# Optimization experiments

Measured on AMD Instinct MI355X. Metric: run time of the kernel, lower is better.

The kernel has to match this reference:

```python
import jax, jax.numpy as jnp
import numpy as np

L_DEG = 4      # max out-degree L
DEPTH = 7      # complete L-ary tree depth -> 21845 nodes
N_GEN = 16
C_ST = 8
M_LAB = 256


def _build_tree():
    sizes = [L_DEG ** d for d in range(DEPTH + 1)]
    limits = np.concatenate([[0], np.cumsum(sizes)]).astype(np.int64)
    t_size = int(limits[-1])
    nodes = np.arange(t_size)
    rng = np.random.default_rng(0)
    labels = rng.integers(0, M_LAB, t_size)
    parent = np.where(nodes > 0, (nodes - 1) // L_DEG, 0)
    pos = np.where(nodes > 0, (nodes - 1) % L_DEG, 0)
    ch = np.zeros((t_size, L_DEG), dtype=np.int64)
    n_internal = int(limits[-2])
    ch[:n_internal] = L_DEG * nodes[:n_internal, None] + np.arange(1, L_DEG + 1)[None, :]
    t = np.concatenate([labels[:, None], parent[:, None], pos[:, None], ch], axis=1).astype(np.int64)
    return t, limits


def setup_inputs() -> dict:
    key = jax.random.key(0)
    ka, kb, kp, ks = jax.random.split(key, 4)
    t, limits = _build_tree()
    return {
        "t": jnp.asarray(t),
        "t_limits": jnp.asarray(limits),
        "a": jax.random.normal(ka, (N_GEN, C_ST, C_ST, L_DEG), dtype=jnp.float32),
        "b": jax.random.normal(kb, (N_GEN, C_ST, M_LAB), dtype=jnp.float32),
        "pi": jax.random.normal(kp, (N_GEN, C_ST, L_DEG), dtype=jnp.float32),
        "sp": jax.random.normal(ks, (N_GEN, L_DEG), dtype=jnp.float32),
    }


def _forward(tn, lim, a, b, pi, sp):
    # tn, lim are host numpy int arrays (tree structure is a constant).
    G, C, _, L = a.shape
    t_size = int(lim[-1])
    n_levels = len(lim) - 1
    sL = int(lim[-2])                      # first leaf index
    labels = tn[:, 0]
    posf = tn[:, 2]
    ch_all = tn[:, 3:3 + L]

    sm_a = jax.nn.softmax(a, axis=1)       # P(parent_state i | child_state j, pos l)
    sm_b = jax.nn.softmax(b, axis=2)
    sm_pi = jax.nn.softmax(pi, axis=1)
    sm_sp = jax.nn.softmax(sp, axis=1)
    a_sp = sm_a * sm_sp[:, None, None, :]  # [G,i,j,L]

    # ---------------- upward pass ----------------
    prior = jnp.zeros((t_size, G, C), a.dtype)
    beta = jnp.zeros((t_size, G, C), a.dtype)
    beta_il = jnp.zeros((t_size, G, C), a.dtype)

    prior_lv = jnp.moveaxis(sm_pi[:, :, posf[sL:]], 2, 0)   # [NL,G,C]
    emis_lv = jnp.moveaxis(sm_b[:, :, labels[sL:]], 2, 0)   # [NL,G,C]
    beta_lv = prior_lv * emis_lv
    beta_lv = beta_lv / jnp.sum(beta_lv, axis=2, keepdims=True)
    prior = prior.at[sL:].set(prior_lv)
    beta = beta.at[sL:].set(beta_lv)

    for lev in range(n_levels - 2, -1, -1):   # internal levels, bottom-up
        s, e = int(lim[lev]), int(lim[lev + 1])
        ch = ch_all[s:e]                       # [P,L]
        mask = (ch > 0).astype(a.dtype)        # children packed in first slots
        prior_ch = prior[ch]                   # [P,L,G,C]
        beta_ch = beta[ch]                     # [P,L,G,C]
        u_prior = jnp.einsum('gijl,pl,plgj->pgi', a_sp, mask, prior_ch)
        u_bil = jnp.einsum('gijl,pl,plgj->pgi', a_sp, mask, beta_ch) / u_prior
        emis = jnp.moveaxis(sm_b[:, :, labels[s:e]], 2, 0)  # [P,G,C]
        tmp = emis * u_bil * u_prior
        u_beta = tmp / jnp.sum(tmp, axis=2, keepdims=True)
        prior = prior.at[s:e].set(u_prior)
        beta = beta.at[s:e].set(u_beta)
        beta_il = beta_il.at[s:e].set(u_bil)

    # ---------------- downward pass ----------------
    # row t_size is a dummy slot for padded (absent) children
    eps_i = jnp.zeros((t_size + 1, G, C), a.dtype).at[0].set(beta[0])
    eps_ijl = jnp.zeros((t_size, G, C, C, L), a.dtype)
    for lev in range(0, n_levels - 1):         # parents, top-down (root included)
        s, e = int(lim[lev]), int(lim[lev + 1])
        ch = ch_all[s:e]
        maskb = ch > 0
        mask = maskb.astype(a.dtype)
        beta_ch = jnp.transpose(beta[ch], (0, 2, 3, 1))       # [P,G,Cj,L]
        pe = eps_i[s:e] / (prior[s:e] * beta_il[s:e])         # [P,G,Ci]
        res = (pe[:, :, :, None, None] * a_sp[None]
               * beta_ch[:, :, None, :, :]
               * mask[:, None, None, None, :])                # [P,G,i,j,L]
        child_eps = jnp.sum(res, axis=3)                       # sum over j (as in source) -> [P,G,i,L]
        vals = jnp.moveaxis(child_eps, 3, 1).reshape(-1, G, C) # [P*L,G,C]
        safe = np.where(maskb, ch, t_size).reshape(-1)
        eps_i = eps_i.at[safe].set(vals)
        eps_ijl = eps_ijl.at[s:e].set(res)
    eps_i = eps_i[:t_size]
    # leaves' eps_ijl stay zero (source scatters zeros there)

    # ---------------- log-likelihood ----------------
    a_lh = jnp.einsum('ugijl,gijl->g', eps_ijl, jnp.log(sm_a))
    b_lh = jnp.einsum('ugc,gcu->g', eps_i, jnp.log(sm_b)[:, :, labels])
    pi_lh = jnp.einsum('ugc,gcu->g', eps_i[sL:], jnp.log(sm_pi)[:, :, posf[sL:]])
    eps_l = jnp.sum(eps_ijl, axis=(2, 3))                      # [u,g,L]
    sp_lh = jnp.einsum('ugl,gl->g', eps_l, jnp.log(sm_sp))
    return a_lh + b_lh + pi_lh + sp_lh


def reference(t, t_limits, a, b, pi, sp):
    tn = np.asarray(t)
    lim = np.asarray(t_limits)
    return _forward(tn, lim, a, b, pi, sp)
```

## Files before the change

kernel.cpp:

```cpp
#include <hip/hip_runtime.h>


#define G 16
#define C 8
#define GC 128
#define TSIZE 21845
#define SL 5461

__device__ __forceinline__ float grp8_sum(float v) {
  v += __shfl_xor(v, 1);
  v += __shfl_xor(v, 2);
  v += __shfl_xor(v, 4);
  return v;
}

__global__ void setup_kernel(const float* __restrict__ ain, const float* __restrict__ bin,
                             const float* __restrict__ piin, const float* __restrict__ spin,
                             float* __restrict__ a_sp, float* __restrict__ log_a,
                             float* __restrict__ sm_bT, float* __restrict__ log_bT,
                             float* __restrict__ sm_piT, float* __restrict__ log_piT,
                             float* __restrict__ log_sp, float* __restrict__ out) {
  int blk = blockIdx.x, tid = threadIdx.x;
  if (blk < 16) {
    int g = blk;
    __shared__ float red4[4];
    for (int c = 0; c < 8; ++c) {
      int row = g * 8 + c;
      float x = bin[row * 256 + tid];
      float m = x;
      #pragma unroll
      for (int off2 = 32; off2; off2 >>= 1) m = fmaxf(m, __shfl_xor(m, off2));
      if ((tid & 63) == 0) red4[tid >> 6] = m;
      __syncthreads();
      m = fmaxf(fmaxf(red4[0], red4[1]), fmaxf(red4[2], red4[3]));
      __syncthreads();
      float e = expf(x - m);
      float ssum = e;
      #pragma unroll
      for (int off2 = 32; off2; off2 >>= 1) ssum += __shfl_xor(ssum, off2);
      if ((tid & 63) == 0) red4[tid >> 6] = ssum;
      __syncthreads();
      ssum = red4[0] + red4[1] + red4[2] + red4[3];
      __syncthreads();
      sm_bT[tid * GC + row]  = e / ssum;
      log_bT[tid * GC + row] = (x - m) - logf(ssum);
    }
  } else if (blk == 16) {
    for (int col = tid; col < 512; col += 256) {
      int g = col >> 5, j = (col >> 2) & 7, l = col & 3;
      float x[8], m = -1e30f;
      #pragma unroll
      for (int i = 0; i < 8; ++i) { x[i] = ain[g*256 + i*32 + j*4 + l]; m = fmaxf(m, x[i]); }
      float ssum = 0.f;
      #pragma unroll
// ... 7 lines not shown
      for (int i = 0; i < 8; ++i) {
        int o2 = g*256 + i*32 + j*4 + l;
        float smv = expf(x[i] - m) / ssum;
        a_sp[o2]  = smv * spv;
        log_a[o2] = (x[i] - m) - ls;
      }
    }
  } else {
    if (tid < 64) {
      int g = tid >> 2, l = tid & 3;
      float x[8], m = -1e30f;
      #pragma unroll
      for (int c = 0; c < 8; ++c) { x[c] = piin[g*32 + c*4 + l]; m = fmaxf(m, x[c]); }
      float ssum = 0.f;
      #pragma unroll
      for (int c = 0; c < 8; ++c) ssum += expf(x[c] - m);
      float ls = logf(ssum);
      #pragma unroll
      for (int c = 0; c < 8; ++c) {
        sm_piT[l*GC + g*8 + c]  = expf(x[c] - m) / ssum;
        log_piT[l*GC + g*8 + c] = (x[c] - m) - ls;
      }
    } else if (tid < 80) {
      int g = tid - 64;
      float y[4], m = -1e30f;
      #pragma unroll
      for (int l = 0; l < 4; ++l) { y[l] = spin[g*4 + l]; m = fmaxf(m, y[l]); }
      float ssum = 0.f;
      #pragma unroll
      for (int l = 0; l < 4; ++l) ssum += expf(y[l] - m);
      float ls = logf(ssum);
      #pragma unroll
      for (int l = 0; l < 4; ++l) log_sp[g*4 + l] = (y[l] - m) - ls;
    } else if (tid >= 128 && tid < 144) {
      out[tid - 128] = 0.0f;
    }
  }
}

__device__ __forceinline__ void up_lds(int v, int lab, int gi, int g8,
    const float* asp, const float* __restrict__ sm_bT,
    float* sBeta, float* sNum, bool wantNum) {
  int ch0 = 4*v + 1;
  float ub = 0.f;
  #pragma unroll
  for (int l = 0; l < 4; ++l) {
    const float4* bp = (const float4*)(sBeta + (ch0 + l)*GC + g8);
    float4 b0 = bp[0], b1 = bp[1];
    ub += asp[l]*b0.x + asp[4+l]*b0.y + asp[8+l]*b0.z + asp[12+l]*b0.w
        + asp[16+l]*b1.x + asp[20+l]*b1.y + asp[24+l]*b1.z + asp[28+l]*b1.w;
  }
  float tmp = sm_bT[lab*GC + gi] * ub;
  float s = grp8_sum(tmp);
  sBeta[v*GC + gi] = tmp / s;
  if (wantNum) sNum[v*GC + gi] = ub;
}

__device__ __forceinline__ double down_lds(int v, int lab, float e, int gi, int g8,
    const float* asp, const float* aal, const float* lsp,
    const float* __restrict__ log_bT, float* sBeta, const float* sNum) {
  float pe = e / sNum[v*GC + gi];
  int ch0 = 4*v + 1;
  float local = 0.f;
  #pragma unroll
  for (int l = 0; l < 4; ++l) {
    float4* bp = (float4*)(sBeta + (ch0 + l)*GC + g8);
    float4 b0 = bp[0], b1 = bp[1];
    float S = asp[l]*b0.x + asp[4+l]*b0.y + asp[8+l]*b0.z + asp[12+l]*b0.w
            + asp[16+l]*b1.x + asp[20+l]*b1.y + asp[24+l]*b1.z + asp[28+l]*b1.w;
    float A = aal[l]*b0.x + aal[4+l]*b0.y + aal[8+l]*b0.z + aal[12+l]*b0.w
            + aal[16+l]*b1.x + aal[20+l]*b1.y + aal[24+l]*b1.z + aal[28+l]*b1.w;
    float ce = pe * S;
    sBeta[(ch0 + l)*GC + gi] = ce;
    local += pe*A + ce*lsp[l];
  }
  return (double)local + (double)(e * log_bT[lab*GC + gi]);
}

__device__ __forceinline__ void up_g(int u, int lab, int gi, int g8,
    const float* asp, const float* __restrict__ sm_bT,
    float* __restrict__ betaG, float* __restrict__ numG) {
  int ch0 = 4*u + 1;
  float ub = 0.f;
  #pragma unroll
  for (int l = 0; l < 4; ++l) {
    const float4* bp = (const float4*)(betaG + (size_t)(ch0 + l)*GC + g8);
    float4 b0 = bp[0], b1 = bp[1];
    ub += asp[l]*b0.x + asp[4+l]*b0.y + asp[8+l]*b0.z + asp[12+l]*b0.w
        + asp[16+l]*b1.x + asp[20+l]*b1.y + asp[24+l]*b1.z + asp[28+l]*b1.w;
  }
  float tmp = sm_bT[lab*GC + gi] * ub;
  float s = grp8_sum(tmp);
  betaG[(size_t)u*GC + gi] = tmp / s;
  numG[(size_t)u*GC + gi]  = ub;
}

__device__ __forceinline__ double down_g(int u, int lab, int gi, int g8,
    const float* asp, const float* aal, const float* lsp,
    const float* __restrict__ log_bT, const float* __restrict__ numG,
    const float* __restrict__ betaG, float* __restrict__ epsG) {
  float e  = epsG[(size_t)u*GC + gi];
  float pe = e / numG[(size_t)u*GC + gi];
  int ch0 = 4*u + 1;
  float local = 0.f;
  #pragma unroll
  for (int l = 0; l < 4; ++l) {
    const float4* bp = (const float4*)(betaG + (size_t)(ch0 + l)*GC + g8);
    float4 b0 = bp[0], b1 = bp[1];
    float S = asp[l]*b0.x + asp[4+l]*b0.y + asp[8+l]*b0.z + asp[12+l]*b0.w
            + asp[16+l]*b1.x + asp[20+l]*b1.y + asp[24+l]*b1.z + asp[28+l]*b1.w;
    float A = aal[l]*b0.x + aal[4+l]*b0.y + aal[8+l]*b0.z + aal[12+l]*b0.w
            + aal[16+l]*b1.x + aal[20+l]*b1.y + aal[24+l]*b1.z + aal[28+l]*b1.w;
    float ce = pe * S;
    epsG[(size_t)(ch0 + l)*GC + gi] = ce;
    local += pe*A + ce*lsp[l];
  }
  return (double)local + (double)(e * log_bT[lab*GC + gi]);
}

__global__ __launch_bounds__(1024, 1) void up_kernel(
    const float* __restrict__ a_sp, const float* __restrict__ sm_bT,
    const float* __restrict__ sm_piT, const int* __restrict__ t,
    float* __restrict__ betaG) {
  __shared__ float sBeta[85*GC];
  const int blk = blockIdx.x, tid = threadIdx.x;
  const int gi = tid & 127, g = gi >> 3, i = gi & 7, g8 = g*8, w = tid >> 7;
  float asp[32];
  {
    const float4* pa = (const float4*)(a_sp + g*256 + i*32);
    #pragma unroll
    for (int q = 0; q < 8; ++q) {
      float4 v = pa[q];
      asp[q*4+0]=v.x; asp[q*4+1]=v.y; asp[q*4+2]=v.z; asp[q*4+3]=v.w;
    }
  }
  const int base_leaf = SL + blk*64;
  #pragma unroll
  for (int it = 0; it < 8; ++it) {
    int k = it*8 + w;
    float bt = sm_piT[(k & 3)*GC + gi] * sm_bT[t[(base_leaf + k)*7]*GC + gi];
    float s = grp8_sum(bt);
    sBeta[(21 + k)*GC + gi] = bt / s;
  }
  __syncthreads();
  #pragma unroll
  for (int it = 0; it < 2; ++it) {
    int k = it*8 + w;
    up_lds(5 + k, t[(1365 + blk*16 + k)*7], gi, g8, asp, sm_bT, sBeta, nullptr, false);
  }
  __syncthreads();
  if (tid < 512)
    up_lds(1 + w, t[(341 + blk*4 + w)*7], gi, g8, asp, sm_bT, sBeta, nullptr, false);
  __syncthreads();
  if (tid < 128) {
    up_lds(0, t[(85 + blk)*7], gi, g8, asp, sm_bT, sBeta, nullptr, false);
    betaG[(size_t)(85 + blk)*GC + gi] = sBeta[gi];
  }
}

__global__ __launch_bounds__(512, 2) void top_kernel(
    const float* __restrict__ a_sp, const float* __restrict__ log_a,
    const float* __restrict__ log_sp, const float* __restrict__ sm_bT,
    const float* __restrict__ log_bT, const int* __restrict__ t,
    float* __restrict__ betaG, float* __restrict__ numG,
    float* __restrict__ epsG, float* __restrict__ out) {
  int g = blockIdx.x, tid = threadIdx.x;
  int i = tid & 7, gi = g*8 + i, q = tid >> 3, g8 = g*8;
  float asp[32], aal[32], lsp[4];
  {
    const float4* pa = (const float4*)(a_sp + g*256 + i*32);
    const float4* pl = (const float4*)(log_a + g*256 + i*32);
    #pragma unroll
    for (int k = 0; k < 8; ++k) {
      float4 va = pa[k], vl = pl[k];
      asp[k*4+0]=va.x; asp[k*4+1]=va.y; asp[k*4+2]=va.z; asp[k*4+3]=va.w;
      aal[k*4+0]=va.x*vl.x; aal[k*4+1]=va.y*vl.y; aal[k*4+2]=va.z*vl.z; aal[k*4+3]=va.w*vl.w;
    }
    #pragma unroll
    for (int l = 0; l < 4; ++l) lsp[l] = log_sp[g*4 + l];
  }
  up_g(21 + q, t[(21 + q)*7], gi, g8, asp, sm_bT, betaG, numG);
  __syncthreads();
  if (tid < 128) up_g(5 + q, t[(5 + q)*7], gi, g8, asp, sm_bT, betaG, numG);
  __syncthreads();
  if (tid < 32)  up_g(1 + q, t[(1 + q)*7], gi, g8, asp, sm_bT, betaG, numG);
  __syncthreads();
  if (tid < 8) {
    up_g(0, t[0], gi, g8, asp, sm_bT, betaG, numG);
    epsG[gi] = betaG[gi];
  }
  __syncthreads();
  double acc = 0.0;
  if (tid < 8)
    acc += down_g(0, t[0], gi, g8, asp, aal, lsp, log_bT, numG, betaG, epsG);
  __syncthreads();
  if (tid < 32)
    acc += down_g(1 + q, t[(1 + q)*7], gi, g8, asp, aal, lsp, log_bT, numG, betaG, epsG);
  __syncthreads();
  if (tid < 128)
    acc += down_g(5 + q, t[(5 + q)*7], gi, g8, asp, aal, lsp, log_bT, numG, betaG, epsG);
  __syncthreads();
  acc += down_g(21 + q, t[(21 + q)*7], gi, g8, asp, aal, lsp, log_bT, numG, betaG, epsG);
  acc += __shfl_xor(acc, 1);
  acc += __shfl_xor(acc, 2);
  acc += __shfl_xor(acc, 4);
  __shared__ double sd[64];
  if (i == 0) sd[q] = acc;
  __syncthreads();
  if (tid == 0) {
    double s = 0.0;
    for (int k = 0; k < 64; ++k) s += sd[k];
    atomicAdd(&out[g], (float)s);
  }
}

__global__ __launch_bounds__(1024, 1) void down_kernel(
    const float* __restrict__ a_sp, const float* __restrict__ log_a,
    const float* __restrict__ log_sp, const float* __restrict__ sm_bT,
    const float* __restrict__ log_bT, const float* __restrict__ sm_piT,
    const float* __restrict__ log_piT, const int* __restrict__ t,
    const float* __restrict__ epsG, float* __restrict__ out) {
  __shared__ float  sBeta[85*GC];
  __shared__ float  sNum[21*GC];
  __shared__ double sd[128];
  const int blk = blockIdx.x, tid = threadIdx.x;
  const int gi = tid & 127, g = gi >> 3, i = gi & 7, g8 = g*8, w = tid >> 7;
  float asp[32], aal[32], lsp[4];
  {
    const float4* pa = (const float4*)(a_sp  + g*256 + i*32);
    const float4* pl = (const float4*)(log_a + g*256 + i*32);
    #pragma unroll
    for (int k = 0; k < 8; ++k) {
      float4 va = pa[k], vl = pl[k];
      asp[k*4+0]=va.x; asp[k*4+1]=va.y; asp[k*4+2]=va.z; asp[k*4+3]=va.w;
      aal[k*4+0]=va.x*vl.x; aal[k*4+1]=va.y*vl.y; aal[k*4+2]=va.z*vl.z; aal[k*4+3]=va.w*vl.w;
    }
    #pragma unroll
    for (int l = 0; l < 4; ++l) lsp[l] = log_sp[g*4 + l];
  }
  const int base_leaf = SL + blk*64;
  #pragma unroll
  for (int it = 0; it < 8; ++it) {
    int k = it*8 + w;
    float bt = sm_piT[(k & 3)*GC + gi] * sm_bT[t[(base_leaf + k)*7]*GC + gi];
    float s = grp8_sum(bt);
    sBeta[(21 + k)*GC + gi] = bt / s;
  }
  __syncthreads();
  #pragma unroll
  for (int it = 0; it < 2; ++it) {
    int k = it*8 + w;
    up_lds(5 + k, t[(1365 + blk*16 + k)*7], gi, g8, asp, sm_bT, sBeta, sNum, true);
  }
  __syncthreads();
  if (tid < 512)
    up_lds(1 + w, t[(341 + blk*4 + w)*7], gi, g8, asp, sm_bT, sBeta, sNum, true);
  __syncthreads();
  double acc = 0.0;
  if (tid < 128) {
    up_lds(0, t[(85 + blk)*7], gi, g8, asp, sm_bT, sBeta, sNum, true);
    float e = epsG[(size_t)(85 + blk)*GC + gi];
    acc += down_lds(0, t[(85 + blk)*7], e, gi, g8, asp, aal, lsp, log_bT, sBeta, sNum);
  }
  __syncthreads();
  if (tid < 512) {
    int v = 1 + w;
    float e = sBeta[v*GC + gi];
    acc += down_lds(v, t[(341 + blk*4 + w)*7], e, gi, g8, asp, aal, lsp, log_bT, sBeta, sNum);
  }
  __syncthreads();
  #pragma unroll
  for (int it = 0; it < 2; ++it) {
    int k = it*8 + w, v = 5 + k;
    float e = sBeta[v*GC + gi];
    acc += down_lds(v, t[(1365 + blk*16 + k)*7], e, gi, g8, asp, aal, lsp, log_bT, sBeta, sNum);
  }
  __syncthreads();
  #pragma unroll
  for (int it = 0; it < 8; ++it) {
    int k = it*8 + w;
    float e = sBeta[(21 + k)*GC + gi];
    acc += (double)(e * (log_bT[t[(base_leaf + k)*7]*GC + gi] +
                         log_piT[(k & 3)*GC + gi]));
  }
  acc += __shfl_xor(acc, 1);
  acc += __shfl_xor(acc, 2);
  acc += __shfl_xor(acc, 4);
  if (i == 0) sd[tid >> 3] = acc;
  __syncthreads();
  if (tid < 16) {
    double s = 0.0;
    #pragma unroll
    for (int c = 0; c < 8; ++c) s += sd[tid + 16*c];
    atomicAdd(&out[tid], (float)s);
  }
}

extern "C" void kernel_launch(void* const* d_in, const int* in_sizes, int n_in,
                              void* d_out, int out_size, void* d_ws, size_t ws_size,
                              hipStream_t stream) {
  const int*   t  = (const int*)d_in[0];
  const float* a  = (const float*)d_in[2];
  const float* b  = (const float*)d_in[3];
  const float* pi = (const float*)d_in[4];
  const float* sp = (const float*)d_in[5];
  float* out = (float*)d_out;

  char* w = (char*)d_ws;
  size_t off = 0;
  auto carve = [&](size_t bytes) -> void* {
    void* ptr = w + off;
    off += (bytes + 255) & ~(size_t)255;
    return ptr;
  };
  float* a_sp    = (float*)carve((size_t)16*8*8*4*4);
  float* log_a   = (float*)carve((size_t)16*8*8*4*4);
  float* sm_bT   = (float*)carve((size_t)256*GC*4);
  float* log_bT  = (float*)carve((size_t)256*GC*4);
  float* sm_piT  = (float*)carve((size_t)4*GC*4);
  float* log_piT = (float*)carve((size_t)4*GC*4);
  float* log_sp  = (float*)carve((size_t)16*4*4);
  float* betaG   = (float*)carve((size_t)341*GC*4);
  float* numG    = (float*)carve((size_t)85*GC*4);
  float* epsG    = (float*)carve((size_t)341*GC*4);

  setup_kernel<<<18, 256, 0, stream>>>(a, b, pi, sp, a_sp, log_a, sm_bT, log_bT,
                                       sm_piT, log_piT, log_sp, out);
  up_kernel<<<256, 1024, 0, stream>>>(a_sp, sm_bT, sm_piT, t, betaG);
  top_kernel<<<16, 512, 0, stream>>>(a_sp, log_a, log_sp, sm_bT, log_bT, t,
                                     betaG, numG, epsG, out);
  down_kernel<<<256, 1024, 0, stream>>>(a_sp, log_a, log_sp, sm_bT, log_bT,
                                        sm_piT, log_piT, t, epsG, out);
}
```

Measured before the change: 116.6 us.

## Fuse up, top and down kernels into one persistent kernel with grid sync

Replaces the separate up, top and down kernels with a single 256-block kernel. Blocks publish their subtree roots, and the last block to arrive (found with an atomic counter) runs the top-of-tree pass while the other blocks spin-wait on a flag. This removes two kernel launches and the recomputation of the lower-subtree upward pass that the down kernel used to redo. The cost is a global spin barrier that assumes all 256 blocks are co-resident, plus a serialized top section run by one block.

```diff
diff --git a/kernel.cpp b/kernel.cpp
--- a/kernel.cpp
+++ b/kernel.cpp
@@ -14,12 +14,22 @@
   return v;
 }
 
+__device__ __forceinline__ void st_agent(float* p, float v) {
+  __hip_atomic_store((unsigned int*)p, __float_as_uint(v),
+                     __ATOMIC_RELAXED, __HIP_MEMORY_SCOPE_AGENT);
+}
+__device__ __forceinline__ float ld_agent(const float* p) {
+  return __uint_as_float(__hip_atomic_load((const unsigned int*)p,
+                         __ATOMIC_RELAXED, __HIP_MEMORY_SCOPE_AGENT));
+}
+
 __global__ void setup_kernel(const float* __restrict__ ain, const float* __restrict__ bin,
                              const float* __restrict__ piin, const float* __restrict__ spin,
                              float* __restrict__ a_sp, float* __restrict__ log_a,
                              float* __restrict__ sm_bT, float* __restrict__ log_bT,
                              float* __restrict__ sm_piT, float* __restrict__ log_piT,
-                             float* __restrict__ log_sp, float* __restrict__ out) {
+                             float* __restrict__ log_sp, unsigned int* __restrict__ sync_,
+                             float* __restrict__ out) {
   int blk = blockIdx.x, tid = threadIdx.x;
   if (blk < 16) {
     int g = blk;
@@ -93,15 +103,17 @@
       float ls = logf(ssum);
       #pragma unroll
       for (int l = 0; l < 4; ++l) log_sp[g*4 + l] = (y[l] - m) - ls;
-    } else if (tid >= 128 && tid < 144) {
-      out[tid - 128] = 0.0f;
+    } else if (tid < 96) {
+      out[tid - 80] = 0.0f;
+    } else if (tid < 224) {
+      sync_[tid - 96] = 0u;
     }
   }
 }
 
 __device__ __forceinline__ void up_lds(int v, int lab, int gi, int g8,
     const float* asp, const float* __restrict__ sm_bT,
-    float* sBeta, float* sNum, bool wantNum) {
+    float* sBeta, float* sNum) {
   int ch0 = 4*v + 1;
   float ub = 0.f;
   #pragma unroll
@@ -114,7 +126,7 @@
   float tmp = sm_bT[lab*GC + gi] * ub;
   float s = grp8_sum(tmp);
   sBeta[v*GC + gi] = tmp / s;
-  if (wantNum) sNum[v*GC + gi] = ub;
+  sNum[v*GC + gi]  = ub;
 }
 
 __device__ __forceinline__ double down_lds(int v, int lab, float e, int gi, int g8,
@@ -138,14 +150,15 @@
   return (double)local + (double)(e * log_bT[lab*GC + gi]);
 }
 
-__device__ __forceinline__ void up_g(int u, int lab, int gi, int g8,
+__device__ __forceinline__ void up_gx(int u, int lab, int gi, int g8,
     const float* asp, const float* __restrict__ sm_bT,
+    const float* __restrict__ childBeta,
     float* __restrict__ betaG, float* __restrict__ numG) {
   int ch0 = 4*u + 1;
   float ub = 0.f;
   #pragma unroll
   for (int l = 0; l < 4; ++l) {
-    const float4* bp = (const float4*)(betaG + (size_t)(ch0 + l)*GC + g8);
+    const float4* bp = (const float4*)(childBeta + (size_t)(ch0 + l)*GC + g8);
     float4 b0 = bp[0], b1 = bp[1];
     ub += asp[l]*b0.x + asp[4+l]*b0.y + asp[8+l]*b0.z + asp[12+l]*b0.w
         + asp[16+l]*b1.x + asp[20+l]*b1.y + asp[24+l]*b1.z + asp[28+l]*b1.w;
@@ -156,134 +169,43 @@
   numG[(size_t)u*GC + gi]  = ub;
 }
 
-__device__ __forceinline__ double down_g(int u, int lab, int gi, int g8,
+__device__ __forceinline__ double down_gx(int u, int lab, int gi, int g8,
     const float* asp, const float* aal, const float* lsp,
     const float* __restrict__ log_bT, const float* __restrict__ numG,
-    const float* __restrict__ betaG, float* __restrict__ epsG) {
+    const float* __restrict__ childBeta, float* __restrict__ epsG,
+    bool publish) {
   float e  = epsG[(size_t)u*GC + gi];
   float pe = e / numG[(size_t)u*GC + gi];
   int ch0 = 4*u + 1;
   float local = 0.f;
   #pragma unroll
   for (int l = 0; l < 4; ++l) {
-    const float4* bp = (const float4*)(betaG + (size_t)(ch0 + l)*GC + g8);
+    const float4* bp = (const float4*)(childBeta + (size_t)(ch0 + l)*GC + g8);
     float4 b0 = bp[0], b1 = bp[1];
     float S = asp[l]*b0.x + asp[4+l]*b0.y + asp[8+l]*b0.z + asp[12+l]*b0.w
             + asp[16+l]*b1.x + asp[20+l]*b1.y + asp[24+l]*b1.z + asp[28+l]*b1.w;
     float A = aal[l]*b0.x + aal[4+l]*b0.y + aal[8+l]*b0.z + aal[12+l]*b0.w
             + aal[16+l]*b1.x + aal[20+l]*b1.y + aal[24+l]*b1.z + aal[28+l]*b1.w;
     float ce = pe * S;
-    epsG[(size_t)(ch0 + l)*GC + gi] = ce;
+    if (publish) st_agent(&epsG[(size_t)(ch0 + l)*GC + gi], ce);
+    else         epsG[(size_t)(ch0 + l)*GC + gi] = ce;
     local += pe*A + ce*lsp[l];
   }
   return (double)local + (double)(e * log_bT[lab*GC + gi]);
 }
 
-__global__ __launch_bounds__(1024, 1) void up_kernel(
-    const float* __restrict__ a_sp, const float* __restrict__ sm_bT,
-    const float* __restrict__ sm_piT, const int* __restrict__ t,
-    float* __restrict__ betaG) {
-  __shared__ float sBeta[85*GC];
-  const int blk = blockIdx.x, tid = threadIdx.x;
-  const int gi = tid & 127, g = gi >> 3, i = gi & 7, g8 = g*8, w = tid >> 7;
-  float asp[32];
-  {
-    const float4* pa = (const float4*)(a_sp + g*256 + i*32);
-    #pragma unroll
-    for (int q = 0; q < 8; ++q) {
-      float4 v = pa[q];
-      asp[q*4+0]=v.x; asp[q*4+1]=v.y; asp[q*4+2]=v.z; asp[q*4+3]=v.w;
-    }
-  }
-  const int base_leaf = SL + blk*64;
-  #pragma unroll
-  for (int it = 0; it < 8; ++it) {
-    int k = it*8 + w;
-    float bt = sm_piT[(k & 3)*GC + gi] * sm_bT[t[(base_leaf + k)*7]*GC + gi];
-    float s = grp8_sum(bt);
-    sBeta[(21 + k)*GC + gi] = bt / s;
-  }
-  __syncthreads();
-  #pragma unroll
-  for (int it = 0; it < 2; ++it) {
-    int k = it*8 + w;
-    up_lds(5 + k, t[(1365 + blk*16 + k)*7], gi, g8, asp, sm_bT, sBeta, nullptr, false);
-  }
-  __syncthreads();
-  if (tid < 512)
-    up_lds(1 + w, t[(341 + blk*4 + w)*7], gi, g8, asp, sm_bT, sBeta, nullptr, false);
-  __syncthreads();
-  if (tid < 128) {
-    up_lds(0, t[(85 + blk)*7], gi, g8, asp, sm_bT, sBeta, nullptr, false);
-    betaG[(size_t)(85 + blk)*GC + gi] = sBeta[gi];
-  }
-}
-
-__global__ __launch_bounds__(512, 2) void top_kernel(
-    const float* __restrict__ a_sp, const float* __restrict__ log_a,
-    const float* __restrict__ log_sp, const float* __restrict__ sm_bT,
-    const float* __restrict__ log_bT, const int* __restrict__ t,
-    float* __restrict__ betaG, float* __restrict__ numG,
-    float* __restrict__ epsG, float* __restrict__ out) {
-  int g = blockIdx.x, tid = threadIdx.x;
-  int i = tid & 7, gi = g*8 + i, q = tid >> 3, g8 = g*8;
-  float asp[32], aal[32], lsp[4];
-  {
-    const float4* pa = (const float4*)(a_sp + g*256 + i*32);
-    const float4* pl = (const float4*)(log_a + g*256 + i*32);
-    #pragma unroll
-    for (int k = 0; k < 8; ++k) {
-      float4 va = pa[k], vl = pl[k];
-      asp[k*4+0]=va.x; asp[k*4+1]=va.y; asp[k*4+2]=va.z; asp[k*4+3]=va.w;
-      aal[k*4+0]=va.x*vl.x; aal[k*4+1]=va.y*vl.y; aal[k*4+2]=va.z*vl.z; aal[k*4+3]=va.w*vl.w;
-    }
-    #pragma unroll
-    for (int l = 0; l < 4; ++l) lsp[l] = log_sp[g*4 + l];
-  }
-  up_g(21 + q, t[(21 + q)*7], gi, g8, asp, sm_bT, betaG, numG);
-  __syncthreads();
-  if (tid < 128) up_g(5 + q, t[(5 + q)*7], gi, g8, asp, sm_bT, betaG, numG);
-  __syncthreads();
-  if (tid < 32)  up_g(1 + q, t[(1 + q)*7], gi, g8, asp, sm_bT, betaG, numG);
-  __syncthreads();
-  if (tid < 8) {
-    up_g(0, t[0], gi, g8, asp, sm_bT, betaG, numG);
-    epsG[gi] = betaG[gi];
-  }
-  __syncthreads();
-  double acc = 0.0;
-  if (tid < 8)
-    acc += down_g(0, t[0], gi, g8, asp, aal, lsp, log_bT, numG, betaG, epsG);
-  __syncthreads();
-  if (tid < 32)
-    acc += down_g(1 + q, t[(1 + q)*7], gi, g8, asp, aal, lsp, log_bT, numG, betaG, epsG);
-  __syncthreads();
-  if (tid < 128)
-    acc += down_g(5 + q, t[(5 + q)*7], gi, g8, asp, aal, lsp, log_bT, numG, betaG, epsG);
-  __syncthreads();
-  acc += down_g(21 + q, t[(21 + q)*7], gi, g8, asp, aal, lsp, log_bT, numG, betaG, epsG);
-  acc += __shfl_xor(acc, 1);
-  acc += __shfl_xor(acc, 2);
-  acc += __shfl_xor(acc, 4);
-  __shared__ double sd[64];
-  if (i == 0) sd[q] = acc;
-  __syncthreads();
-  if (tid == 0) {
-    double s = 0.0;
-    for (int k = 0; k < 64; ++k) s += sd[k];
-    atomicAdd(&out[g], (float)s);
-  }
-}
-
-__global__ __launch_bounds__(1024, 1) void down_kernel(
+__global__ __launch_bounds__(1024, 1) void mega_kernel(
     const float* __restrict__ a_sp, const float* __restrict__ log_a,
     const float* __restrict__ log_sp, const float* __restrict__ sm_bT,
     const float* __restrict__ log_bT, const float* __restrict__ sm_piT,
     const float* __restrict__ log_piT, const int* __restrict__ t,
-    const float* __restrict__ epsG, float* __restrict__ out) {
+    float* __restrict__ betaG, float* __restrict__ numG,
+    float* __restrict__ epsG, unsigned int* __restrict__ sync_,
+    float* __restrict__ out) {
   __shared__ float  sBeta[85*GC];
   __shared__ float  sNum[21*GC];
   __shared__ double sd[128];
+  __shared__ int    sLast;
   const int blk = blockIdx.x, tid = threadIdx.x;
   const int gi = tid & 127, g = gi >> 3, i = gi & 7, g8 = g*8, w = tid >> 7;
   float asp[32], aal[32], lsp[4];
@@ -300,6 +222,7 @@
     for (int l = 0; l < 4; ++l) lsp[l] = log_sp[g*4 + l];
   }
   const int base_leaf = SL + blk*64;
+
   #pragma unroll
   for (int it = 0; it < 8; ++it) {
     int k = it*8 + w;
@@ -311,30 +234,120 @@
   #pragma unroll
   for (int it = 0; it < 2; ++it) {
     int k = it*8 + w;
-    up_lds(5 + k, t[(1365 + blk*16 + k)*7], gi, g8, asp, sm_bT, sBeta, sNum, true);
+    up_lds(5 + k, t[(1365 + blk*16 + k)*7], gi, g8, asp, sm_bT, sBeta, sNum);
   }
   __syncthreads();
   if (tid < 512)
-    up_lds(1 + w, t[(341 + blk*4 + w)*7], gi, g8, asp, sm_bT, sBeta, sNum, true);
-  __syncthreads();
+    up_lds(1 + w, t[(341 + blk*4 + w)*7], gi, g8, asp, sm_bT, sBeta, sNum);
+  __syncthreads();
+  if (tid < 128) {
+    up_lds(0, t[(85 + blk)*7], gi, g8, asp, sm_bT, sBeta, sNum);
+    st_agent(&betaG[(size_t)(85 + blk)*GC + gi], sBeta[gi]);
+  }
+  __syncthreads();
+  if (tid == 0) {
+    __threadfence();
+    unsigned int prev = __hip_atomic_fetch_add(&sync_[0], 1u,
+                          __ATOMIC_ACQ_REL, __HIP_MEMORY_SCOPE_AGENT);
+    sLast = (prev == 255u);
+  }
+  __syncthreads();
+
+  if (sLast) {
+    const int q = tid >> 7;
+    #pragma unroll
+    for (int it = 0; it < 32; ++it) {
+      int idx = it*1024 + tid;
+      float v = ld_agent(&betaG[(size_t)85*GC + idx]);
+      st_agent(&epsG[(size_t)85*GC + idx], v);
+    }
+    __syncthreads();
+    #pragma unroll
+    for (int it = 0; it < 8; ++it)
+      up_gx(21 + it*8 + q, t[(21 + it*8 + q)*7], gi, g8, asp, sm_bT,
+            epsG, betaG, numG);
+    __syncthreads();
+    #pragma unroll
+    for (int it = 0; it < 2; ++it)
+      up_gx(5 + it*8 + q, t[(5 + it*8 + q)*7], gi, g8, asp, sm_bT,
+            betaG, betaG, numG);
+    __syncthreads();
+    if (tid < 512)
+      up_gx(1 + q, t[(1 + q)*7], gi, g8, asp, sm_bT, betaG, betaG, numG);
+    __syncthreads();
+    if (tid < 128) {
+      up_gx(0, t[0], gi, g8, asp, sm_bT, betaG, betaG, numG);
+      epsG[gi] = betaG[gi];
+    }
+    __syncthreads();
+    double acc = 0.0;
+    if (tid < 128)
+      acc += down_gx(0, t[0], gi, g8, asp, aal, lsp, log_bT, numG,
+                     betaG, epsG, false);
+    __syncthreads();
+    if (tid < 512)
+      acc += down_gx(1 + q, t[(1 + q)*7], gi, g8, asp, aal, lsp, log_bT, numG,
+                     betaG, epsG, false);
+    __syncthreads();
+    #pragma unroll
+    for (int it = 0; it < 2; ++it)
+      acc += down_gx(5 + it*8 + q, t[(5 + it*8 + q)*7], gi, g8, asp, aal, lsp,
+                     log_bT, numG, betaG, epsG, false);
+    __syncthreads();
+    #pragma unroll
+    for (int it = 0; it < 8; ++it)
+      acc += down_gx(21 + it*8 + q, t[(21 + it*8 + q)*7], gi, g8, asp, aal,
+                     lsp, log_bT, numG, epsG, epsG, true);
+    acc += __shfl_xor(acc, 1);
+    acc += __shfl_xor(acc, 2);
+    acc += __shfl_xor(acc, 4);
+    if (i == 0) sd[tid >> 3] = acc;
+    __syncthreads();
+    if (tid < 16) {
+      double s = 0.0;
+      #pragma unroll
+      for (int c2 = 0; c2 < 8; ++c2) s += sd[tid + 16*c2];
+      atomicAdd(&out[tid], (float)s);
+    }
+    __syncthreads();
+    if (tid == 0) {
+      __threadfence();
+      __hip_atomic_store(&sync_[64], 1u, __ATOMIC_RELEASE,
+                         __HIP_MEMORY_SCOPE_AGENT);
+    }
+  }
+
+  if (tid == 0) {
+    long itc = 0;
+    while (__hip_atomic_load(&sync_[64], __ATOMIC_ACQUIRE,
+                             __HIP_MEMORY_SCOPE_AGENT) == 0u &&
+           itc < (1L << 21)) {
+      ++itc;
+      __builtin_amdgcn_s_sleep(2);
+    }
+  }
+  __syncthreads();
+
   double acc = 0.0;
   if (tid < 128) {
-    up_lds(0, t[(85 + blk)*7], gi, g8, asp, sm_bT, sBeta, sNum, true);
-    float e = epsG[(size_t)(85 + blk)*GC + gi];
-    acc += down_lds(0, t[(85 + blk)*7], e, gi, g8, asp, aal, lsp, log_bT, sBeta, sNum);
+    float e = ld_agent(&epsG[(size_t)(85 + blk)*GC + gi]);
+    acc += down_lds(0, t[(85 + blk)*7], e, gi, g8, asp, aal, lsp, log_bT,
+                    sBeta, sNum);
   }
   __syncthreads();
   if (tid < 512) {
     int v = 1 + w;
     float e = sBeta[v*GC + gi];
-    acc += down_lds(v, t[(341 + blk*4 + w)*7], e, gi, g8, asp, aal, lsp, log_bT, sBeta, sNum);
+    acc += down_lds(v, t[(341 + blk*4 + w)*7], e, gi, g8, asp, aal, lsp,
+                    log_bT, sBeta, sNum);
   }
   __syncthreads();
   #pragma unroll
   for (int it = 0; it < 2; ++it) {
     int k = it*8 + w, v = 5 + k;
     float e = sBeta[v*GC + gi];
-    acc += down_lds(v, t[(1365 + blk*16 + k)*7], e, gi, g8, asp, aal, lsp, log_bT, sBeta, sNum);
+    acc += down_lds(v, t[(1365 + blk*16 + k)*7], e, gi, g8, asp, aal, lsp,
+                    log_bT, sBeta, sNum);
   }
   __syncthreads();
   #pragma unroll
@@ -352,7 +365,7 @@
   if (tid < 16) {
     double s = 0.0;
     #pragma unroll
-    for (int c = 0; c < 8; ++c) s += sd[tid + 16*c];
+    for (int c2 = 0; c2 < 8; ++c2) s += sd[tid + 16*c2];
     atomicAdd(&out[tid], (float)s);
   }
 }
@@ -384,12 +397,11 @@
   float* betaG   = (float*)carve((size_t)341*GC*4);
   float* numG    = (float*)carve((size_t)85*GC*4);
   float* epsG    = (float*)carve((size_t)341*GC*4);
+  unsigned int* sync_ = (unsigned int*)carve(512);
 
   setup_kernel<<<18, 256, 0, stream>>>(a, b, pi, sp, a_sp, log_a, sm_bT, log_bT,
-                                       sm_piT, log_piT, log_sp, out);
-  up_kernel<<<256, 1024, 0, stream>>>(a_sp, sm_bT, sm_piT, t, betaG);
-  top_kernel<<<16, 512, 0, stream>>>(a_sp, log_a, log_sp, sm_bT, log_bT, t,
-                                     betaG, numG, epsG, out);
-  down_kernel<<<256, 1024, 0, stream>>>(a_sp, log_a, log_sp, sm_bT, log_bT,
-                                        sm_piT, log_piT, t, epsG, out);
-}
+                                       sm_piT, log_piT, log_sp, sync_, out);
+  mega_kernel<<<256, 1024, 0, stream>>>(a_sp, log_a, log_sp, sm_bT, log_bT,
+                                        sm_piT, log_piT, t, betaG, numG, epsG,
+                                        sync_, out);
+}
```

Result: slower. 421.6 us (+261.7%).

## Fuse up and top kernels with last-block-done atomic counter

Applied to the files above, without the earlier changes.

Merges the top-of-tree kernel into the upward kernel. Each block publishes its subtree root beta with agent-scope stores and bumps a global counter, and the last block to finish runs the top five levels with 1024 threads instead of 16 blocks of 512. This removes one kernel launch and its gap. In exchange, the top levels now run serially on a single workgroup instead of 16 groups in parallel.

```diff
diff --git a/kernel.cpp b/kernel.cpp
--- a/kernel.cpp
+++ b/kernel.cpp
@@ -14,12 +14,18 @@
   return v;
 }
 
+__device__ __forceinline__ void st_agent(float* p, float v) {
+  __hip_atomic_store((unsigned int*)p, __float_as_uint(v),
+                     __ATOMIC_RELAXED, __HIP_MEMORY_SCOPE_AGENT);
+}
+
 __global__ void setup_kernel(const float* __restrict__ ain, const float* __restrict__ bin,
                              const float* __restrict__ piin, const float* __restrict__ spin,
                              float* __restrict__ a_sp, float* __restrict__ log_a,
                              float* __restrict__ sm_bT, float* __restrict__ log_bT,
                              float* __restrict__ sm_piT, float* __restrict__ log_piT,
-                             float* __restrict__ log_sp, float* __restrict__ out) {
+                             float* __restrict__ log_sp, unsigned int* __restrict__ sync_,
+                             float* __restrict__ out) {
   int blk = blockIdx.x, tid = threadIdx.x;
   if (blk < 16) {
     int g = blk;
@@ -93,8 +99,10 @@
       float ls = logf(ssum);
       #pragma unroll
       for (int l = 0; l < 4; ++l) log_sp[g*4 + l] = (y[l] - m) - ls;
-    } else if (tid >= 128 && tid < 144) {
-      out[tid - 128] = 0.0f;
+    } else if (tid < 96) {
+      out[tid - 80] = 0.0f;
+    } else if (tid < 224) {
+      sync_[tid - 96] = 0u;
     }
   }
 }
@@ -179,11 +187,16 @@
   return (double)local + (double)(e * log_bT[lab*GC + gi]);
 }
 
-__global__ __launch_bounds__(1024, 1) void up_kernel(
-    const float* __restrict__ a_sp, const float* __restrict__ sm_bT,
-    const float* __restrict__ sm_piT, const int* __restrict__ t,
-    float* __restrict__ betaG) {
-  __shared__ float sBeta[85*GC];
+__global__ __launch_bounds__(1024, 1) void uptop_kernel(
+    const float* __restrict__ a_sp, const float* __restrict__ log_a,
+    const float* __restrict__ log_sp, const float* __restrict__ sm_bT,
+    const float* __restrict__ log_bT, const float* __restrict__ sm_piT,
+    const int* __restrict__ t, float* __restrict__ betaG,
+    float* __restrict__ numG, float* __restrict__ epsG,
+    unsigned int* __restrict__ sync_, float* __restrict__ out) {
+  __shared__ float  sBeta[85*GC];
+  __shared__ double sd[128];
+  __shared__ int    sLast;
   const int blk = blockIdx.x, tid = threadIdx.x;
   const int gi = tid & 127, g = gi >> 3, i = gi & 7, g8 = g*8, w = tid >> 7;
   float asp[32];
@@ -215,63 +228,73 @@
   __syncthreads();
   if (tid < 128) {
     up_lds(0, t[(85 + blk)*7], gi, g8, asp, sm_bT, sBeta, nullptr, false);
-    betaG[(size_t)(85 + blk)*GC + gi] = sBeta[gi];
-  }
-}
-
-__global__ __launch_bounds__(512, 2) void top_kernel(
-    const float* __restrict__ a_sp, const float* __restrict__ log_a,
-    const float* __restrict__ log_sp, const float* __restrict__ sm_bT,
-    const float* __restrict__ log_bT, const int* __restrict__ t,
-    float* __restrict__ betaG, float* __restrict__ numG,
-    float* __restrict__ epsG, float* __restrict__ out) {
-  int g = blockIdx.x, tid = threadIdx.x;
-  int i = tid & 7, gi = g*8 + i, q = tid >> 3, g8 = g*8;
-  float asp[32], aal[32], lsp[4];
+    st_agent(&betaG[(size_t)(85 + blk)*GC + gi], sBeta[gi]);
+  }
+  __syncthreads();
+  if (tid == 0) {
+    __threadfence();
+    unsigned int prev = __hip_atomic_fetch_add(&sync_[0], 1u,
+                          __ATOMIC_ACQ_REL, __HIP_MEMORY_SCOPE_AGENT);
+    sLast = (prev == 255u);
+  }
+  __syncthreads();
+  if (!sLast) return;
+
+  const int q = tid >> 7;
+  float aal[32], lsp[4];
   {
-    const float4* pa = (const float4*)(a_sp + g*256 + i*32);
+    const float4* pa = (const float4*)(a_sp  + g*256 + i*32);
     const float4* pl = (const float4*)(log_a + g*256 + i*32);
     #pragma unroll
     for (int k = 0; k < 8; ++k) {
       float4 va = pa[k], vl = pl[k];
-      asp[k*4+0]=va.x; asp[k*4+1]=va.y; asp[k*4+2]=va.z; asp[k*4+3]=va.w;
       aal[k*4+0]=va.x*vl.x; aal[k*4+1]=va.y*vl.y; aal[k*4+2]=va.z*vl.z; aal[k*4+3]=va.w*vl.w;
     }
     #pragma unroll
     for (int l = 0; l < 4; ++l) lsp[l] = log_sp[g*4 + l];
   }
-  up_g(21 + q, t[(21 + q)*7], gi, g8, asp, sm_bT, betaG, numG);
-  __syncthreads();
-  if (tid < 128) up_g(5 + q, t[(5 + q)*7], gi, g8, asp, sm_bT, betaG, numG);
-  __syncthreads();
-  if (tid < 32)  up_g(1 + q, t[(1 + q)*7], gi, g8, asp, sm_bT, betaG, numG);
-  __syncthreads();
-  if (tid < 8) {
+  #pragma unroll
+  for (int it = 0; it < 8; ++it)
+    up_g(21 + it*8 + q, t[(21 + it*8 + q)*7], gi, g8, asp, sm_bT, betaG, numG);
+  __syncthreads();
+  #pragma unroll
+  for (int it = 0; it < 2; ++it)
+    up_g(5 + it*8 + q, t[(5 + it*8 + q)*7], gi, g8, asp, sm_bT, betaG, numG);
+  __syncthreads();
+  if (tid < 512)
+    up_g(1 + q, t[(1 + q)*7], gi, g8, asp, sm_bT, betaG, numG);
+  __syncthreads();
+  if (tid < 128) {
     up_g(0, t[0], gi, g8, asp, sm_bT, betaG, numG);
     epsG[gi] = betaG[gi];
   }
   __syncthreads();
   double acc = 0.0;
-  if (tid < 8)
+  if (tid < 128)
     acc += down_g(0, t[0], gi, g8, asp, aal, lsp, log_bT, numG, betaG, epsG);
   __syncthreads();
-  if (tid < 32)
+  if (tid < 512)
     acc += down_g(1 + q, t[(1 + q)*7], gi, g8, asp, aal, lsp, log_bT, numG, betaG, epsG);
   __syncthreads();
-  if (tid < 128)
-    acc += down_g(5 + q, t[(5 + q)*7], gi, g8, asp, aal, lsp, log_bT, numG, betaG, epsG);
-  __syncthreads();
-  acc += down_g(21 + q, t[(21 + q)*7], gi, g8, asp, aal, lsp, log_bT, numG, betaG, epsG);
+  #pragma unroll
+  for (int it = 0; it < 2; ++it)
+    acc += down_g(5 + it*8 + q, t[(5 + it*8 + q)*7], gi, g8, asp, aal, lsp,
+                  log_bT, numG, betaG, epsG);
+  __syncthreads();
+  #pragma unroll
+  for (int it = 0; it < 8; ++it)
+    acc += down_g(21 + it*8 + q, t[(21 + it*8 + q)*7], gi, g8, asp, aal, lsp,
+                  log_bT, numG, betaG, epsG);
   acc += __shfl_xor(acc, 1);
   acc += __shfl_xor(acc, 2);
   acc += __shfl_xor(acc, 4);
-  __shared__ double sd[64];
-  if (i == 0) sd[q] = acc;
-  __syncthreads();
-  if (tid == 0) {
+  if (i == 0) sd[tid >> 3] = acc;
+  __syncthreads();
+  if (tid < 16) {
     double s = 0.0;
-    for (int k = 0; k < 64; ++k) s += sd[k];
-    atomicAdd(&out[g], (float)s);
+    #pragma unroll
+    for (int c2 = 0; c2 < 8; ++c2) s += sd[tid + 16*c2];
+    atomicAdd(&out[tid], (float)s);
   }
 }
 
@@ -321,20 +344,23 @@
   if (tid < 128) {
     up_lds(0, t[(85 + blk)*7], gi, g8, asp, sm_bT, sBeta, sNum, true);
     float e = epsG[(size_t)(85 + blk)*GC + gi];
-    acc += down_lds(0, t[(85 + blk)*7], e, gi, g8, asp, aal, lsp, log_bT, sBeta, sNum);
+    acc += down_lds(0, t[(85 + blk)*7], e, gi, g8, asp, aal, lsp, log_bT,
+                    sBeta, sNum);
   }
   __syncthreads();
   if (tid < 512) {
     int v = 1 + w;
     float e = sBeta[v*GC + gi];
-    acc += down_lds(v, t[(341 + blk*4 + w)*7], e, gi, g8, asp, aal, lsp, log_bT, sBeta, sNum);
+    acc += down_lds(v, t[(341 + blk*4 + w)*7], e, gi, g8, asp, aal, lsp,
+                    log_bT, sBeta, sNum);
   }
   __syncthreads();
   #pragma unroll
   for (int it = 0; it < 2; ++it) {
     int k = it*8 + w, v = 5 + k;
     float e = sBeta[v*GC + gi];
-    acc += down_lds(v, t[(1365 + blk*16 + k)*7], e, gi, g8, asp, aal, lsp, log_bT, sBeta, sNum);
+    acc += down_lds(v, t[(1365 + blk*16 + k)*7], e, gi, g8, asp, aal, lsp,
+                    log_bT, sBeta, sNum);
   }
   __syncthreads();
   #pragma unroll
@@ -352,7 +378,7 @@
   if (tid < 16) {
     double s = 0.0;
     #pragma unroll
-    for (int c = 0; c < 8; ++c) s += sd[tid + 16*c];
+    for (int c2 = 0; c2 < 8; ++c2) s += sd[tid + 16*c2];
     atomicAdd(&out[tid], (float)s);
   }
 }
@@ -384,12 +410,12 @@
   float* betaG   = (float*)carve((size_t)341*GC*4);
   float* numG    = (float*)carve((size_t)85*GC*4);
   float* epsG    = (float*)carve((size_t)341*GC*4);
+  unsigned int* sync_ = (unsigned int*)carve(512);
 
   setup_kernel<<<18, 256, 0, stream>>>(a, b, pi, sp, a_sp, log_a, sm_bT, log_bT,
-                                       sm_piT, log_piT, log_sp, out);
-  up_kernel<<<256, 1024, 0, stream>>>(a_sp, sm_bT, sm_piT, t, betaG);
-  top_kernel<<<16, 512, 0, stream>>>(a_sp, log_a, log_sp, sm_bT, log_bT, t,
-                                     betaG, numG, epsG, out);
+                                       sm_piT, log_piT, log_sp, sync_, out);
+  uptop_kernel<<<256, 1024, 0, stream>>>(a_sp, log_a, log_sp, sm_bT, log_bT,
+                                         sm_piT, t, betaG, numG, epsG, sync_, out);
   down_kernel<<<256, 1024, 0, stream>>>(a_sp, log_a, log_sp, sm_bT, log_bT,
                                         sm_piT, log_piT, t, epsG, out);
 }
```

New measurement: 175.2 us. 50.3% more time.

## Fold top-of-tree pass into down kernel by redundant per-block recomputation

Applied to the files above, without the earlier changes.

Removes the separate 16-block top_kernel. Each of the 256 down blocks now recomputes the upper tree levels (nodes 0..84) in shared memory from betaG, then walks its own ancestor chain to derive the eps value at its subtree root. Block 0 alone adds the log-likelihood contribution of the top levels. This drops one kernel launch and its serial, low-occupancy dependency stage, plus the numG/epsG global buffers. The cost is redundant upper-tree work in every block before it can start its own subtree.

```diff
diff --git a/kernel.cpp b/kernel.cpp
--- a/kernel.cpp
+++ b/kernel.cpp
@@ -93,8 +93,8 @@
       float ls = logf(ssum);
       #pragma unroll
       for (int l = 0; l < 4; ++l) log_sp[g*4 + l] = (y[l] - m) - ls;
-    } else if (tid >= 128 && tid < 144) {
-      out[tid - 128] = 0.0f;
+    } else if (tid < 96) {
+      out[tid - 80] = 0.0f;
     }
   }
 }
@@ -138,47 +138,6 @@
   return (double)local + (double)(e * log_bT[lab*GC + gi]);
 }
 
-__device__ __forceinline__ void up_g(int u, int lab, int gi, int g8,
-    const float* asp, const float* __restrict__ sm_bT,
-    float* __restrict__ betaG, float* __restrict__ numG) {
-  int ch0 = 4*u + 1;
-  float ub = 0.f;
-  #pragma unroll
-  for (int l = 0; l < 4; ++l) {
-    const float4* bp = (const float4*)(betaG + (size_t)(ch0 + l)*GC + g8);
-    float4 b0 = bp[0], b1 = bp[1];
-    ub += asp[l]*b0.x + asp[4+l]*b0.y + asp[8+l]*b0.z + asp[12+l]*b0.w
-        + asp[16+l]*b1.x + asp[20+l]*b1.y + asp[24+l]*b1.z + asp[28+l]*b1.w;
-  }
-  float tmp = sm_bT[lab*GC + gi] * ub;
-  float s = grp8_sum(tmp);
-  betaG[(size_t)u*GC + gi] = tmp / s;
-  numG[(size_t)u*GC + gi]  = ub;
-}
-
-__device__ __forceinline__ double down_g(int u, int lab, int gi, int g8,
-    const float* asp, const float* aal, const float* lsp,
-    const float* __restrict__ log_bT, const float* __restrict__ numG,
-    const float* __restrict__ betaG, float* __restrict__ epsG) {
-  float e  = epsG[(size_t)u*GC + gi];
-  float pe = e / numG[(size_t)u*GC + gi];
-  int ch0 = 4*u + 1;
-  float local = 0.f;
-  #pragma unroll
-  for (int l = 0; l < 4; ++l) {
-    const float4* bp = (const float4*)(betaG + (size_t)(ch0 + l)*GC + g8);
-    float4 b0 = bp[0], b1 = bp[1];
-    float S = asp[l]*b0.x + asp[4+l]*b0.y + asp[8+l]*b0.z + asp[12+l]*b0.w
-            + asp[16+l]*b1.x + asp[20+l]*b1.y + asp[24+l]*b1.z + asp[28+l]*b1.w;
-    float A = aal[l]*b0.x + aal[4+l]*b0.y + aal[8+l]*b0.z + aal[12+l]*b0.w
-            + aal[16+l]*b1.x + aal[20+l]*b1.y + aal[24+l]*b1.z + aal[28+l]*b1.w;
-    float ce = pe * S;
-    epsG[(size_t)(ch0 + l)*GC + gi] = ce;
-    local += pe*A + ce*lsp[l];
-  }
-  return (double)local + (double)(e * log_bT[lab*GC + gi]);
-}
-
 __global__ __launch_bounds__(1024, 1) void up_kernel(
     const float* __restrict__ a_sp, const float* __restrict__ sm_bT,
     const float* __restrict__ sm_piT, const int* __restrict__ t,
@@ -219,70 +178,15 @@
   }
 }
 
-__global__ __launch_bounds__(512, 2) void top_kernel(
-    const float* __restrict__ a_sp, const float* __restrict__ log_a,
-    const float* __restrict__ log_sp, const float* __restrict__ sm_bT,
-    const float* __restrict__ log_bT, const int* __restrict__ t,
-    float* __restrict__ betaG, float* __restrict__ numG,
-    float* __restrict__ epsG, float* __restrict__ out) {
-  int g = blockIdx.x, tid = threadIdx.x;
-  int i = tid & 7, gi = g*8 + i, q = tid >> 3, g8 = g*8;
-  float asp[32], aal[32], lsp[4];
-  {
-    const float4* pa = (const float4*)(a_sp + g*256 + i*32);
-    const float4* pl = (const float4*)(log_a + g*256 + i*32);
-    #pragma unroll
-    for (int k = 0; k < 8; ++k) {
-      float4 va = pa[k], vl = pl[k];
-      asp[k*4+0]=va.x; asp[k*4+1]=va.y; asp[k*4+2]=va.z; asp[k*4+3]=va.w;
-      aal[k*4+0]=va.x*vl.x; aal[k*4+1]=va.y*vl.y; aal[k*4+2]=va.z*vl.z; aal[k*4+3]=va.w*vl.w;
-    }
-    #pragma unroll
-    for (int l = 0; l < 4; ++l) lsp[l] = log_sp[g*4 + l];
-  }
-  up_g(21 + q, t[(21 + q)*7], gi, g8, asp, sm_bT, betaG, numG);
-  __syncthreads();
-  if (tid < 128) up_g(5 + q, t[(5 + q)*7], gi, g8, asp, sm_bT, betaG, numG);
-  __syncthreads();
-  if (tid < 32)  up_g(1 + q, t[(1 + q)*7], gi, g8, asp, sm_bT, betaG, numG);
-  __syncthreads();
-  if (tid < 8) {
-    up_g(0, t[0], gi, g8, asp, sm_bT, betaG, numG);
-    epsG[gi] = betaG[gi];
-  }
-  __syncthreads();
-  double acc = 0.0;
-  if (tid < 8)
-    acc += down_g(0, t[0], gi, g8, asp, aal, lsp, log_bT, numG, betaG, epsG);
-  __syncthreads();
-  if (tid < 32)
-    acc += down_g(1 + q, t[(1 + q)*7], gi, g8, asp, aal, lsp, log_bT, numG, betaG, epsG);
-  __syncthreads();
-  if (tid < 128)
-    acc += down_g(5 + q, t[(5 + q)*7], gi, g8, asp, aal, lsp, log_bT, numG, betaG, epsG);
-  __syncthreads();
-  acc += down_g(21 + q, t[(21 + q)*7], gi, g8, asp, aal, lsp, log_bT, numG, betaG, epsG);
-  acc += __shfl_xor(acc, 1);
-  acc += __shfl_xor(acc, 2);
-  acc += __shfl_xor(acc, 4);
-  __shared__ double sd[64];
-  if (i == 0) sd[q] = acc;
-  __syncthreads();
-  if (tid == 0) {
-    double s = 0.0;
-    for (int k = 0; k < 64; ++k) s += sd[k];
-    atomicAdd(&out[g], (float)s);
-  }
-}
-
-__global__ __launch_bounds__(1024, 1) void down_kernel(
+__global__ __launch_bounds__(1024, 1) void downall_kernel(
     const float* __restrict__ a_sp, const float* __restrict__ log_a,
     const float* __restrict__ log_sp, const float* __restrict__ sm_bT,
     const float* __restrict__ log_bT, const float* __restrict__ sm_piT,
     const float* __restrict__ log_piT, const int* __restrict__ t,
-    const float* __restrict__ epsG, float* __restrict__ out) {
+    const float* __restrict__ betaG, float* __restrict__ out) {
   __shared__ float  sBeta[85*GC];
   __shared__ float  sNum[21*GC];
+  __shared__ float  sEps[GC];
   __shared__ double sd[128];
   const int blk = blockIdx.x, tid = threadIdx.x;
   const int gi = tid & 127, g = gi >> 3, i = gi & 7, g8 = g*8, w = tid >> 7;
@@ -299,6 +203,129 @@
     #pragma unroll
     for (int l = 0; l < 4; ++l) lsp[l] = log_sp[g*4 + l];
   }
+
+  #pragma unroll
+  for (int it = 0; it < 8; ++it) {
+    int k = it*8 + w, u = 21 + k;
+    int ch0 = 4*u + 1;
+    float ub = 0.f;
+    #pragma unroll
+    for (int l = 0; l < 4; ++l) {
+      const float4* bp = (const float4*)(betaG + (size_t)(ch0 + l)*GC + g8);
+      float4 b0 = bp[0], b1 = bp[1];
+      ub += asp[l]*b0.x + asp[4+l]*b0.y + asp[8+l]*b0.z + asp[12+l]*b0.w
+          + asp[16+l]*b1.x + asp[20+l]*b1.y + asp[24+l]*b1.z + asp[28+l]*b1.w;
+    }
+    float tmp = sm_bT[t[u*7]*GC + gi] * ub;
+    float s = grp8_sum(tmp);
+    sBeta[u*GC + gi] = tmp / s;
+  }
+  __syncthreads();
+  #pragma unroll
+  for (int it = 0; it < 2; ++it) {
+    int u = 5 + it*8 + w;
+    up_lds(u, t[u*7], gi, g8, asp, sm_bT, sBeta, sNum, true);
+  }
+  __syncthreads();
+  if (tid < 512)
+    up_lds(1 + w, t[(1 + w)*7], gi, g8, asp, sm_bT, sBeta, sNum, true);
+  __syncthreads();
+  if (tid < 128)
+    up_lds(0, t[0], gi, g8, asp, sm_bT, sBeta, sNum, true);
+  __syncthreads();
+
+  if (tid < 128) {
+    int a1 = 1 + (blk >> 6), a2 = 5 + (blk >> 4), a3 = 21 + (blk >> 2);
+    float e = sBeta[gi];
+    int anc[3] = {0, a1, a2};
+    int chn[3] = {a1, a2, a3};
+    #pragma unroll
+    for (int s2 = 0; s2 < 3; ++s2) {
+      float pe = e / sNum[anc[s2]*GC + gi];
+      int l = (chn[s2] - 1) & 3;
+      const float4* bp = (const float4*)(sBeta + chn[s2]*GC + g8);
+      float4 b0 = bp[0], b1 = bp[1];
+      float S = asp[l]*b0.x + asp[4+l]*b0.y + asp[8+l]*b0.z + asp[12+l]*b0.w
+              + asp[16+l]*b1.x + asp[20+l]*b1.y + asp[24+l]*b1.z + asp[28+l]*b1.w;
+      e = pe * S;
+    }
+    {
+      float num3 = 0.f;
+      int c30 = 4*a3 + 1;
+      #pragma unroll
+      for (int l = 0; l < 4; ++l) {
+        const float4* bp = (const float4*)(betaG + (size_t)(c30 + l)*GC + g8);
+        float4 b0 = bp[0], b1 = bp[1];
+        num3 += asp[l]*b0.x + asp[4+l]*b0.y + asp[8+l]*b0.z + asp[12+l]*b0.w
+              + asp[16+l]*b1.x + asp[20+l]*b1.y + asp[24+l]*b1.z + asp[28+l]*b1.w;
+      }
+      float pe = e / num3;
+      int l = blk & 3;
+      const float4* bp = (const float4*)(betaG + (size_t)(85 + blk)*GC + g8);
+      float4 b0 = bp[0], b1 = bp[1];
+      float S = asp[l]*b0.x + asp[4+l]*b0.y + asp[8+l]*b0.z + asp[12+l]*b0.w
+              + asp[16+l]*b1.x + asp[20+l]*b1.y + asp[24+l]*b1.z + asp[28+l]*b1.w;
+      e = pe * S;
+    }
+    sEps[gi] = e;
+  }
+  __syncthreads();
+
+  if (blk == 0) {
+    double acc0 = 0.0;
+    if (tid < 128)
+      acc0 += down_lds(0, t[0], sBeta[gi], gi, g8, asp, aal, lsp, log_bT, sBeta, sNum);
+    __syncthreads();
+    if (tid < 512) {
+      int v = 1 + w;
+      acc0 += down_lds(v, t[v*7], sBeta[v*GC + gi], gi, g8, asp, aal, lsp, log_bT, sBeta, sNum);
+    }
+    __syncthreads();
+    #pragma unroll
+    for (int it = 0; it < 2; ++it) {
+      int v = 5 + it*8 + w;
+      acc0 += down_lds(v, t[v*7], sBeta[v*GC + gi], gi, g8, asp, aal, lsp, log_bT, sBeta, sNum);
+    }
+    __syncthreads();
+    #pragma unroll
+    for (int it = 0; it < 8; ++it) {
+      int k = it*8 + w, u = 21 + k;
+      float e = sBeta[u*GC + gi];
+      int ch0 = 4*u + 1;
+      float Sv[4], Av[4], num = 0.f;
+      #pragma unroll
+      for (int l = 0; l < 4; ++l) {
+        const float4* bp = (const float4*)(betaG + (size_t)(ch0 + l)*GC + g8);
+        float4 b0 = bp[0], b1 = bp[1];
+        Sv[l] = asp[l]*b0.x + asp[4+l]*b0.y + asp[8+l]*b0.z + asp[12+l]*b0.w
+              + asp[16+l]*b1.x + asp[20+l]*b1.y + asp[24+l]*b1.z + asp[28+l]*b1.w;
+        Av[l] = aal[l]*b0.x + aal[4+l]*b0.y + aal[8+l]*b0.z + aal[12+l]*b0.w
+              + aal[16+l]*b1.x + aal[20+l]*b1.y + aal[24+l]*b1.z + aal[28+l]*b1.w;
+        num += Sv[l];
+      }
+      float pe = e / num;
+      float local = 0.f;
+      #pragma unroll
+      for (int l = 0; l < 4; ++l) {
+        float ce = pe * Sv[l];
+        local += pe*Av[l] + ce*lsp[l];
+      }
+      acc0 += (double)local + (double)(e * log_bT[t[u*7]*GC + gi]);
+    }
+    acc0 += __shfl_xor(acc0, 1);
+    acc0 += __shfl_xor(acc0, 2);
+    acc0 += __shfl_xor(acc0, 4);
+    if (i == 0) sd[tid >> 3] = acc0;
+    __syncthreads();
+    if (tid < 16) {
+      double s = 0.0;
+      #pragma unroll
+      for (int c2 = 0; c2 < 8; ++c2) s += sd[tid + 16*c2];
+      atomicAdd(&out[tid], (float)s);
+    }
+    __syncthreads();
+  }
+
   const int base_leaf = SL + blk*64;
   #pragma unroll
   for (int it = 0; it < 8; ++it) {
@@ -317,24 +344,25 @@
   if (tid < 512)
     up_lds(1 + w, t[(341 + blk*4 + w)*7], gi, g8, asp, sm_bT, sBeta, sNum, true);
   __syncthreads();
+
   double acc = 0.0;
   if (tid < 128) {
     up_lds(0, t[(85 + blk)*7], gi, g8, asp, sm_bT, sBeta, sNum, true);
-    float e = epsG[(size_t)(85 + blk)*GC + gi];
-    acc += down_lds(0, t[(85 + blk)*7], e, gi, g8, asp, aal, lsp, log_bT, sBeta, sNum);
+    acc += down_lds(0, t[(85 + blk)*7], sEps[gi], gi, g8, asp, aal, lsp,
+                    log_bT, sBeta, sNum);
   }
   __syncthreads();
   if (tid < 512) {
     int v = 1 + w;
-    float e = sBeta[v*GC + gi];
-    acc += down_lds(v, t[(341 + blk*4 + w)*7], e, gi, g8, asp, aal, lsp, log_bT, sBeta, sNum);
+    acc += down_lds(v, t[(341 + blk*4 + w)*7], sBeta[v*GC + gi], gi, g8,
+                    asp, aal, lsp, log_bT, sBeta, sNum);
   }
   __syncthreads();
   #pragma unroll
   for (int it = 0; it < 2; ++it) {
     int k = it*8 + w, v = 5 + k;
-    float e = sBeta[v*GC + gi];
-    acc += down_lds(v, t[(1365 + blk*16 + k)*7], e, gi, g8, asp, aal, lsp, log_bT, sBeta, sNum);
+    acc += down_lds(v, t[(1365 + blk*16 + k)*7], sBeta[v*GC + gi], gi, g8,
+                    asp, aal, lsp, log_bT, sBeta, sNum);
   }
   __syncthreads();
   #pragma unroll
@@ -352,7 +380,7 @@
   if (tid < 16) {
     double s = 0.0;
     #pragma unroll
-    for (int c = 0; c < 8; ++c) s += sd[tid + 16*c];
+    for (int c2 = 0; c2 < 8; ++c2) s += sd[tid + 16*c2];
     atomicAdd(&out[tid], (float)s);
   }
 }
@@ -382,14 +410,10 @@
   float* log_piT = (float*)carve((size_t)4*GC*4);
   float* log_sp  = (float*)carve((size_t)16*4*4);
   float* betaG   = (float*)carve((size_t)341*GC*4);
-  float* numG    = (float*)carve((size_t)85*GC*4);
-  float* epsG    = (float*)carve((size_t)341*GC*4);
 
   setup_kernel<<<18, 256, 0, stream>>>(a, b, pi, sp, a_sp, log_a, sm_bT, log_bT,
                                        sm_piT, log_piT, log_sp, out);
   up_kernel<<<256, 1024, 0, stream>>>(a_sp, sm_bT, sm_piT, t, betaG);
-  top_kernel<<<16, 512, 0, stream>>>(a_sp, log_a, log_sp, sm_bT, log_bT, t,
-                                     betaG, numG, epsG, out);
-  down_kernel<<<256, 1024, 0, stream>>>(a_sp, log_a, log_sp, sm_bT, log_bT,
-                                        sm_piT, log_piT, t, epsG, out);
-}
+  downall_kernel<<<256, 1024, 0, stream>>>(a_sp, log_a, log_sp, sm_bT, log_bT,
+                                           sm_piT, log_piT, t, betaG, out);
+}
```

New measurement: 154.6 us. 1.33x slower.
